# Performance work log

Hardware: AMD Instinct MI355X
Metric: run time of the kernel (lower is better)

## Reference

```python
import jax, jax.numpy as jnp
import numpy as np

K = 9          # neighbors per node (loop=False)
BN_EPS = 1e-5  # BatchNorm2d eps


def setup_inputs() -> dict:
    key = jax.random.key(0)
    k1, k2, k3 = jax.random.split(key, 3)
    B, C, H, W_ = 16, 384, 32, 32
    x = jax.random.normal(k1, (B, C, H, W_), dtype=jnp.float32)
    # GCNConv linear weight (PyG stores [out, in]; y = x @ W.T) and bias
    Wg = jax.random.normal(k2, (C, C), dtype=jnp.float32) / np.sqrt(C)
    bg = jax.random.normal(k3, (C,), dtype=jnp.float32) * 0.02
    gamma = jnp.ones((C,), dtype=jnp.float32)
    beta = jnp.zeros((C,), dtype=jnp.float32)
    return {"x": x, "Wg": Wg, "bg": bg, "gamma": gamma, "beta": beta}


def _knn_indices(xn):
    # xn: [B, N, C] -> neighbor indices [B, N, K] (self excluded)
    sq = jnp.sum(xn * xn, axis=-1)                       # [B, N]
    d = sq[:, :, None] + sq[:, None, :] - 2.0 * jnp.einsum("bnc,bmc->bnm", xn, xn)
    N = xn.shape[1]
    d = d + jnp.eye(N, dtype=xn.dtype) * jnp.finfo(xn.dtype).max  # exclude self
    _, nbr = jax.lax.top_k(-d, K)                        # [B, N, K]
    return nbr


def reference(x, Wg, bg, gamma, beta):
    B, C, H, W_ = x.shape
    N = H * W_
    BN_nodes = B * N
    shortcut = x

    # Flatten to nodes: [B*N, C]
    xn = jnp.transpose(x, (0, 2, 3, 1)).reshape(B, N, C)

    # Per-graph kNN in feature space (PyG knn_graph, flow source_to_target:
    # edges from neighbor (src) to query node (dst))
    nbr = _knn_indices(xn)                                # [B, N, K]
    offs = (jnp.arange(B) * N)[:, None, None]             # [B,1,1]
    src = (nbr + offs).reshape(-1)                        # [B*N*K]
    dst = jnp.broadcast_to(jnp.arange(N)[None, :, None] + offs, (B, N, K)).reshape(-1)

    # GCNConv: add self loops, symmetric normalization
    loops = jnp.arange(BN_nodes)
    src = jnp.concatenate([src, loops])
    dst = jnp.concatenate([dst, loops])

    xw = xn.reshape(BN_nodes, C) @ Wg.T                   # node-wise linear

    deg = jax.ops.segment_sum(jnp.ones_like(dst, dtype=xw.dtype), dst, num_segments=BN_nodes)
    dinv = jax.lax.rsqrt(deg)                             # deg >= 1 due to self loops
    norm = dinv[src] * dinv[dst]                          # [E]

    out = jax.ops.segment_sum(norm[:, None] * xw[src], dst, num_segments=BN_nodes) + bg

    # Back to B x C x H x W
    out = jnp.transpose(out.reshape(B, H, W_, C), (0, 3, 1, 2))

    # BatchNorm2d (training-mode batch statistics, biased variance)
    mu = jnp.mean(out, axis=(0, 2, 3), keepdims=True)
    var = jnp.mean((out - mu) ** 2, axis=(0, 2, 3), keepdims=True)
    out = gamma[None, :, None, None] * (out - mu) * jax.lax.rsqrt(var + BN_EPS) + beta[None, :, None, None]

    # GELU + residual (drop_path = 0 -> identity)
    out = jax.nn.gelu(out) + shortcut
    return out
```

## Files before the change

### kernel.cpp

```cpp
#include <hip/hip_runtime.h>
#include <math.h>

#define B_ 16
#define C_ 384
#define N_ 1024
#define K_ 9

typedef _Float16 f16x8 __attribute__((ext_vector_type(8)));
typedef _Float16 f16x4 __attribute__((ext_vector_type(4)));
typedef float f32x4 __attribute__((ext_vector_type(4)));
typedef unsigned long long u64;

__device__ __forceinline__ void gld_lds16(const void* g, void* l) {
  __builtin_amdgcn_global_load_lds((const __attribute__((address_space(1))) void*)g,
                                   (__attribute__((address_space(3))) void*)l, 16, 0, 0);
}

__global__ __launch_bounds__(256) void k_cvt(const float* __restrict__ x,
                                             const float* __restrict__ Wg,
                                             ushort* __restrict__ xhT, ushort* __restrict__ xlT,
                                             float* __restrict__ sq, ushort* __restrict__ WgH,
                                             ushort* __restrict__ WgL,
                                             float* __restrict__ stats) {
  const int bid = blockIdx.x;
  const int t = threadIdx.x;
  if (bid >= 512) {
    const int i = ((bid - 512) * 256 + t) * 4;
    float4 v = *(const float4*)(Wg + i);
    float vv[4] = {v.x, v.y, v.z, v.w};
    f16x4 hv, lv;
#pragma unroll
    for (int j = 0; j < 4; ++j) {
      _Float16 h = (_Float16)vv[j];
      hv[j] = h;
      lv[j] = (_Float16)(vv[j] - (float)h);
    }
    *(f16x4*)(WgH + i) = hv;
    *(f16x4*)(WgL + i) = lv;
    if (bid == 512) {
      stats[t] = 0.f;
      stats[t + 256] = 0.f;
      stats[t + 512] = 0.f;
    }
    return;
  }
  const int b = bid >> 5, n0 = (bid & 31) * 32;
  __shared__ float ld[384 * 33];
  {
    const int cb = t >> 2, j8 = (t & 3) * 8;
#pragma unroll
    for (int i = 0; i < 6; ++i) {
      const int c = i * 64 + cb;
      const float* src = x + ((size_t)(b * C_ + c) * N_ + n0 + j8);
      float4 v0 = *(const float4*)src;
      float4 v1 = *(const float4*)(src + 4);
      float* dst = &ld[c * 33 + j8];
      dst[0] = v0.x; dst[1] = v0.y; dst[2] = v0.z; dst[3] = v0.w;
      dst[4] = v1.x; dst[5] = v1.y; dst[6] = v1.z; dst[7] = v1.w;
    }
  }
  __syncthreads();
  {
    const int n = t >> 3, l = t & 7;
#pragma unroll
    for (int i = 0; i < 6; ++i) {
      const int c8 = i * 64 + l * 8;
      f16x8 hv, lv;
#pragma unroll
      for (int j = 0; j < 8; ++j) {
        float v = ld[(c8 + j) * 33 + n];
        _Float16 h = (_Float16)v;
        hv[j] = h;
        lv[j] = (_Float16)(v - (float)h);
      }
      const size_t off = (size_t)(b * N_ + n0 + n) * C_ + c8;
      *(f16x8*)(xhT + off) = hv;
      *(f16x8*)(xlT + off) = lv;
    }
    double s = 0.0;
    const int cbase = l * 48;
#pragma unroll
    for (int cc = 0; cc < 48; ++cc) {
      float v = ld[(cbase + cc) * 33 + n];
      s = fma((double)v, (double)v, s);
    }
    s += __shfl_xor(s, 1, 64);
    s += __shfl_xor(s, 2, 64);
    s += __shfl_xor(s, 4, 64);
    if (l == 0) sq[b * N_ + n0 + n] = (float)s;
  }
}

__device__ __forceinline__ void ce2f(float& a, float& b) {
  float lo = fminf(a, b), hi = fmaxf(a, b);
  a = lo;
  b = hi;
}
__device__ __forceinline__ void ce9u(u64& a, u64& b) {
  u64 lo = a < b ? a : b;
  u64 hi = a < b ? b : a;
  a = lo;
  b = hi;
}
__device__ __forceinline__ void mrg9(float* a, const float* b) {
  float m[9];
#pragma unroll
  for (int k = 0; k < 9; ++k) m[k] = fminf(a[k], b[8 - k]);
  ce2f(m[0], m[8]);
  ce2f(m[1], m[5]); ce2f(m[2], m[6]); ce2f(m[3], m[7]); ce2f(m[4], m[8]);
  ce2f(m[1], m[3]); ce2f(m[2], m[4]); ce2f(m[5], m[7]); ce2f(m[6], m[8]);
  ce2f(m[1], m[2]); ce2f(m[3], m[4]); ce2f(m[5], m[6]); ce2f(m[7], m[8]);
#pragma unroll
  for (int k = 0; k < 9; ++k) a[k] = m[k];
}

__global__ __launch_bounds__(256, 2) void k_gx(const ushort* __restrict__ xhT,
                                               const ushort* __restrict__ xlT,
                                               const float* __restrict__ sq,
                                               u64* __restrict__ part,
                                               const ushort* __restrict__ WgH,
                                               const ushort* __restrict__ WgL,
                                               float* __restrict__ xw) {
  __shared__ alignas(16) char sm[2][32768];
  const int bid = blockIdx.x;
  const int t = threadIdx.x;
  const int lane = t & 63, wid = t >> 6, quad = lane >> 4, lrow = lane & 15;
  const int wr = wid >> 1, wc = wid & 1;
  const int lrow4 = lane >> 2, lpos = lane & 3;

  if (bid >= 576) {
    const int bid2 = bid - 576;
    const int xcd = bid2 & 7, j = bid2 >> 3;
    const int pair = xcd * 16 + j / 6;
    const int ct = j % 6;
    const int b = pair >> 3, nt = pair & 7;
    const int co0 = ct * 64, n0 = nt * 128;
    char* smbase = &sm[0][0];

    f32x4 acc[2][4];
#pragma unroll
    for (int mi = 0; mi < 2; ++mi)
#pragma unroll
      for (int ni = 0; ni < 4; ++ni) acc[mi][ni] = (f32x4){0.f, 0.f, 0.f, 0.f};

    const char* asrc[2] = {(const char*)(WgH + (size_t)co0 * C_),
                           (const char*)(WgL + (size_t)co0 * C_)};
    const char* bsrc[2] = {(const char*)(xhT + (size_t)(b * N_ + n0) * C_),
                           (const char*)(xlT + (size_t)(b * N_ + n0) * C_)};

    auto stage = [&](int it) {
      char* dst = smbase + (it & 1) * 24576;
      const int ktB = it * 64;
#pragma unroll
      for (int i = 0; i < 6; ++i) {
        const int c = wid * 6 + i;
        const char* src;
        int base, row;
        if (c < 8) {
          const int arr = c >> 2, sub = c & 3;
          src = asrc[arr];
          base = arr * 4096 + sub * 1024;
          row = sub * 16 + lrow4;
        } else {
          const int cc = c - 8, arr = cc >> 3, sub = cc & 7;
          src = bsrc[arr];
          base = 8192 + arr * 8192 + sub * 1024;
          row = sub * 16 + lrow4;
        }
        const int swz = lpos ^ ((row >> 1) & 3);
        gld_lds16(src + (size_t)row * 768 + ktB + swz * 16, dst + base + lane * 16);
      }
    };

    stage(0);
    for (int it = 0; it < 12; ++it) {
      __syncthreads();
      if (it < 11) stage(it + 1);
      const char* smb = smbase + (it & 1) * 24576;
      f16x8 bh[4], bl[4];
#pragma unroll
      for (int ni = 0; ni < 4; ++ni) {
        const int row = wr * 64 + ni * 16 + lrow;
        const int off = row * 64 + (quad ^ ((row >> 1) & 3)) * 16;
        bh[ni] = *(const f16x8*)(smb + 8192 + off);
        bl[ni] = *(const f16x8*)(smb + 16384 + off);
      }
#pragma unroll
      for (int mi = 0; mi < 2; ++mi) {
        const int row = wc * 32 + mi * 16 + lrow;
        const int off = row * 64 + (quad ^ ((row >> 1) & 3)) * 16;
        f16x8 ah = *(const f16x8*)(smb + off);
        f16x8 al = *(const f16x8*)(smb + 4096 + off);
#pragma unroll
        for (int ni = 0; ni < 4; ++ni) {
          acc[mi][ni] = __builtin_amdgcn_mfma_f32_16x16x32_f16(ah, bh[ni], acc[mi][ni], 0, 0, 0);
          acc[mi][ni] = __builtin_amdgcn_mfma_f32_16x16x32_f16(al, bh[ni], acc[mi][ni], 0, 0, 0);
          acc[mi][ni] = __builtin_amdgcn_mfma_f32_16x16x32_f16(ah, bl[ni], acc[mi][ni], 0, 0, 0);
        }
      }
    }
#pragma unroll
    for (int mi = 0; mi < 2; ++mi)
#pragma unroll
      for (int ni = 0; ni < 4; ++ni)
#pragma unroll
        for (int r = 0; r < 4; ++r) {
          const int c_g = co0 + wc * 32 + mi * 16 + quad * 4 + r;
          const int n_g = n0 + wr * 64 + ni * 16 + lrow;
          xw[((size_t)b * C_ + c_g) * N_ + n_g] = acc[mi][ni][r];
        }
    return;
  }

  const int xcd = bid & 7, j = bid >> 3;
  const int b_local = xcd * 2 + j / 36;
  int pid = j % 36;
  int rt = 0, off0 = 0;
  while (pid >= off0 + (8 - rt)) {
    off0 += 8 - rt;
    ++rt;
  }
  const int mt = rt + (pid - off0);
  const int b = b_local;
  const int n0 = rt * 128, m0 = mt * 128;

  const char* src = (const char*)((wid & 1) ? xlT : xhT) +
                    (size_t)(b * N_ + ((wid >> 1) ? m0 : n0)) * C_ * 2;

  f32x4 acc[4][4];
#pragma unroll
  for (int mi = 0; mi < 4; ++mi)
#pragma unroll
    for (int ni = 0; ni < 4; ++ni) acc[mi][ni] = (f32x4){0.f, 0.f, 0.f, 0.f};

  auto stage = [&](int it) {
    char* dst = sm[it & 1] + wid * 8192;
    const int ktB = it * 64;
#pragma unroll
    for (int i = 0; i < 8; ++i) {
      const int row = i * 16 + lrow4;
      const int swz = lpos ^ ((row >> 1) & 3);
      gld_lds16(src + (size_t)row * 768 + ktB + swz * 16, dst + i * 1024 + lane * 16);
    }
  };

  stage(0);
  for (int it = 0; it < 12; ++it) {
    __syncthreads();
    if (it < 11) stage(it + 1);
    const char* smb = sm[it & 1];
    f16x8 ah[4], al[4];
#pragma unroll
    for (int mi = 0; mi < 4; ++mi) {
      const int row = wr * 64 + mi * 16 + lrow;
      const int off = row * 64 + (quad ^ ((row >> 1) & 3)) * 16;
      ah[mi] = *(const f16x8*)(smb + off);
      al[mi] = *(const f16x8*)(smb + 8192 + off);
    }
#pragma unroll
    for (int ni = 0; ni < 4; ++ni) {
      const int row = wc * 64 + ni * 16 + lrow;
      const int off = row * 64 + (quad ^ ((row >> 1) & 3)) * 16;
      f16x8 bh = *(const f16x8*)(smb + 16384 + off);
      f16x8 bl = *(const f16x8*)(smb + 24576 + off);
#pragma unroll
      for (int mi = 0; mi < 4; ++mi) {
        acc[mi][ni] = __builtin_amdgcn_mfma_f32_16x16x32_f16(bh, ah[mi], acc[mi][ni], 0, 0, 0);
        acc[mi][ni] = __builtin_amdgcn_mfma_f32_16x16x32_f16(bh, al[mi], acc[mi][ni], 0, 0, 0);
        acc[mi][ni] = __builtin_amdgcn_mfma_f32_16x16x32_f16(bl, ah[mi], acc[mi][ni], 0, 0, 0);
      }
    }
  }
  __syncthreads();

  const float* sqb = sq + b * N_;
  float sqm_[4][4];
#pragma unroll
  for (int ni = 0; ni < 4; ++ni)
#pragma unroll
    for (int r = 0; r < 4; ++r) sqm_[ni][r] = sqb[m0 + wc * 64 + ni * 16 + quad * 4 + r];
  float sqq_[4];
#pragma unroll
  for (int mi = 0; mi < 4; ++mi) sqq_[mi] = sqb[n0 + wr * 64 + mi * 16 + lrow];

  float* smf = (float*)sm;
#pragma unroll
  for (int mi = 0; mi < 4; ++mi) {
    const int qL = wr * 64 + mi * 16 + lrow;
    const int qG = n0 + qL;
#pragma unroll
    for (int ni = 0; ni < 4; ++ni) {
      const int tc = wc * 16 + ni * 4 + quad;
      const int stv = tc ^ (qL & 31);
      f32x4 dv;
#pragma unroll
      for (int r = 0; r < 4; ++r) {
        const int mG = m0 + wc * 64 + ni * 16 + quad * 4 + r;
        float d = fmaf(-2.f, acc[mi][ni][r], sqq_[mi] + sqm_[ni][r]);
        if (mG == qG) d = 3.402823466e38f;
        dv[r] = d;
      }
      *(f32x4*)(smf + qL * 128 + stv * 4) = dv;
    }
  }
  __syncthreads();

  const int half = lane >> 5;
  float kA[9], kB[9], kC[9], kD[9];

  {
    const int qsel = wid * 32 + (lane & 31);
#pragma unroll
    for (int k = 0; k < 9; ++k) kA[k] = kB[k] = kC[k] = kD[k] = 3.402823466e38f;
    auto ins16 = [&](float* key, int tcb) {
#pragma unroll
      for (int i = 0; i < 4; ++i) {
        const int tc = tcb + i;
        const int stv = tc ^ (qsel & 31);
        f32x4 q4 = *(const f32x4*)(smf + qsel * 128 + stv * 4);
#pragma unroll
        for (int e = 0; e < 4; ++e) {
          key[8] = fminf(key[8], q4[e]);
#pragma unroll
          for (int s = 8; s >= 1; --s) ce2f(key[s - 1], key[s]);
        }
      }
    };
    ins16(kA, half * 16 + 0);
    ins16(kB, half * 16 + 4);
    ins16(kC, half * 16 + 8);
    ins16(kD, half * 16 + 12);
    mrg9(kA, kB);
    mrg9(kC, kD);
    mrg9(kA, kC);
    {
      float pk[9];
#pragma unroll
      for (int k = 0; k < 9; ++k) pk[k] = __shfl_xor(kA[k], 32, 64);
      mrg9(kA, pk);
    }
    const float v9 = kA[8];
    int c_lt = 0;
#pragma unroll
    for (int k = 0; k < 8; ++k) c_lt += (kA[k] < v9) ? 1 : 0;

    u64 lt_mask = 0ull, eq_mask = 0ull;
#pragma unroll
    for (int i = 0; i < 16; ++i) {
      const int tc = half * 16 + i;
      const int stv = tc ^ (qsel & 31);
      f32x4 q4 = *(const f32x4*)(smf + qsel * 128 + stv * 4);
#pragma unroll
      for (int e = 0; e < 4; ++e) {
        const int jj = i * 4 + e;
        lt_mask |= (q4[e] < v9) ? (1ull << jj) : 0ull;
        eq_mask |= (q4[e] == v9) ? (1ull << jj) : 0ull;
      }
    }
    const int ltc = __popcll(lt_mask), eqc = __popcll(eq_mask);
    const int packed = ltc | (eqc << 16);
    const int other = __shfl_xor(packed, 32, 64);
    const int lt_pref = half ? (other & 0xFFFF) : 0;
    const int eq_pref = half ? (other >> 16) : 0;

    u64* pp = part + (((size_t)(b_local * 8 + mt) * N_) + (n0 + qsel)) * 9;
    int slot = lt_pref;
    u64 msk = lt_mask;
    while (msk) {
      const int jj = __builtin_ctzll(msk);
      msk &= msk - 1;
      const int mL = half * 64 + jj;
      const int stv = (mL >> 2) ^ (qsel & 31);
      const float val = smf[qsel * 128 + stv * 4 + (mL & 3)];
      unsigned fb = __float_as_uint(val);
      unsigned mono = (fb >> 31) ? ~fb : (fb | 0x80000000u);
      pp[slot++] = ((u64)mono << 32) | (unsigned)(m0 + mL);
    }
    unsigned fb9 = __float_as_uint(v9);
    unsigned mono9 = (fb9 >> 31) ? ~fb9 : (fb9 | 0x80000000u);
    slot = c_lt + eq_pref;
    msk = eq_mask;
    while (msk && slot < 9) {
      const int jj = __builtin_ctzll(msk);
      msk &= msk - 1;
      pp[slot++] = ((u64)mono9 << 32) | (unsigned)(m0 + half * 64 + jj);
    }
  }

  if (rt != mt) {
    const int msel = wid * 32 + (lane & 31);
    const int mlo = msel & 3, mhi = msel >> 2;
#pragma unroll
    for (int k = 0; k < 9; ++k) kA[k] = kB[k] = kC[k] = kD[k] = 3.402823466e38f;
    auto insCol = [&](float* key, int q0) {
#pragma unroll
      for (int i = 0; i < 16; ++i) {
        const int qL = q0 + i;
        const float v = smf[qL * 128 + ((mhi ^ (qL & 31)) << 2) + mlo];
        key[8] = fminf(key[8], v);
#pragma unroll
        for (int s = 8; s >= 1; --s) ce2f(key[s - 1], key[s]);
      }
    };
    insCol(kA, half * 64 + 0);
    insCol(kB, half * 64 + 16);
    insCol(kC, half * 64 + 32);
    insCol(kD, half * 64 + 48);
    mrg9(kA, kB);
    mrg9(kC, kD);
    mrg9(kA, kC);
    {
      float pk[9];
#pragma unroll
      for (int k = 0; k < 9; ++k) pk[k] = __shfl_xor(kA[k], 32, 64);
      mrg9(kA, pk);
    }
    const float v9 = kA[8];
    int c_lt = 0;
#pragma unroll
    for (int k = 0; k < 8; ++k) c_lt += (kA[k] < v9) ? 1 : 0;

    u64 lt_mask = 0ull, eq_mask = 0ull;
#pragma unroll
    for (int jj = 0; jj < 64; ++jj) {
      const int qL = half * 64 + jj;
      const float v = smf[qL * 128 + ((mhi ^ (qL & 31)) << 2) + mlo];
      lt_mask |= (v < v9) ? (1ull << jj) : 0ull;
      eq_mask |= (v == v9) ? (1ull << jj) : 0ull;
    }
    const int ltc = __popcll(lt_mask), eqc = __popcll(eq_mask);
    const int packed = ltc | (eqc << 16);
    const int other = __shfl_xor(packed, 32, 64);
    const int lt_pref = half ? (other & 0xFFFF) : 0;
    const int eq_pref = half ? (other >> 16) : 0;

    u64* pp = part + (((size_t)(b_local * 8 + rt) * N_) + (m0 + msel)) * 9;
    int slot = lt_pref;
    u64 msk = lt_mask;
    while (msk) {
      const int jj = __builtin_ctzll(msk);
      msk &= msk - 1;
      const int qL = half * 64 + jj;
      const float val = smf[qL * 128 + ((mhi ^ (qL & 31)) << 2) + mlo];
      unsigned fb = __float_as_uint(val);
      unsigned mono = (fb >> 31) ? ~fb : (fb | 0x80000000u);
      pp[slot++] = ((u64)mono << 32) | (unsigned)(n0 + qL);
    }
    unsigned fb9 = __float_as_uint(v9);
    unsigned mono9 = (fb9 >> 31) ? ~fb9 : (fb9 | 0x80000000u);
    slot = c_lt + eq_pref;
    msk = eq_mask;
    while (msk && slot < 9) {
      const int jj = __builtin_ctzll(msk);
      msk &= msk - 1;
      pp[slot++] = ((u64)mono9 << 32) | (unsigned)(n0 + half * 64 + jj);
    }
  }
}

__global__ void k_mrg(const u64* __restrict__ part, int* __restrict__ nbr, int base_node) {
  const int nl = blockIdx.x * 256 + threadIdx.x;
  const int bl = nl >> 10, q = nl & 1023;
  const u64* p = part + ((size_t)(bl * 8) * N_ + q) * 9;
  u64 key[9];
#pragma unroll
  for (int k = 0; k < 9; ++k) key[k] = ~0ull;
#pragma unroll
  for (int seg = 0; seg < 8; ++seg) {
    const u64* ps = p + (size_t)seg * N_ * 9;
#pragma unroll
    for (int k9 = 0; k9 < 9; ++k9) {
      u64 kk = ps[k9];
      key[8] = key[8] < kk ? key[8] : kk;
#pragma unroll
      for (int s = 8; s >= 1; --s) ce9u(key[s - 1], key[s]);
    }
  }
  int* np = nbr + (size_t)(base_node + nl) * K_;
#pragma unroll
  for (int k = 0; k < 9; ++k) np[k] = (int)(unsigned)(key[k] & 0xFFFFFFFFu);
}

__global__ __launch_bounds__(256) void k_agg(const float* __restrict__ xw,
                                             const int* __restrict__ nbr,
                                             const float* __restrict__ bg,
                                             float* __restrict__ out,
                                             float* __restrict__ stats) {
  const int ct = blockIdx.x % (C_ / 8);
  const int b = blockIdx.x / (C_ / 8);
  const int c0 = ct * 8;
  __shared__ alignas(16) int nb_l[N_ * K_];
  __shared__ alignas(16) float row_l[8][N_ + 4];
  __shared__ float red[2][8][4];
  const int tid = threadIdx.x;
  const int4* gp = (const int4*)(nbr + (size_t)b * N_ * K_);
  int4* lp = (int4*)nb_l;
  for (int t = tid; t < N_ * K_ / 4; t += 256) lp[t] = gp[t];
  for (int t = tid; t < 8 * (N_ / 4); t += 256) {
    const int j = t >> 8, n4 = t & 255;
    float4 v = ((const float4*)(xw + ((size_t)(b * C_ + c0 + j)) * N_))[n4];
    *(float4*)&row_l[j][n4 * 4] = v;
  }
  __syncthreads();
  float bgc[8];
#pragma unroll
  for (int j = 0; j < 8; ++j) bgc[j] = bg[c0 + j];
  float s1[8], s2[8];
#pragma unroll
  for (int j = 0; j < 8; ++j) {
    s1[j] = 0.f;
    s2[j] = 0.f;
  }
  float* outb = out + ((size_t)b * C_ + c0) * N_;
#pragma unroll
  for (int s = 0; s < 4; ++s) {
    const int n = tid + 256 * s;
    const int* nn_ = &nb_l[n * K_];
    int idx[K_];
#pragma unroll
    for (int k = 0; k < K_; ++k) idx[k] = nn_[k];
    float a[8];
#pragma unroll
    for (int j = 0; j < 8; ++j) a[j] = row_l[j][n];
#pragma unroll
    for (int k = 0; k < K_; ++k) {
      const int m = idx[k];
#pragma unroll
      for (int j = 0; j < 8; ++j) a[j] += row_l[j][m];
    }
#pragma unroll
    for (int j = 0; j < 8; ++j) {
      float y = fmaf(a[j], 0.099999994f, bgc[j]);
      outb[(size_t)j * N_ + n] = y;
      s1[j] += y;
      s2[j] = fmaf(y, y, s2[j]);
    }
  }
#pragma unroll
  for (int off = 32; off > 0; off >>= 1)
#pragma unroll
    for (int j = 0; j < 8; ++j) {
      s1[j] += __shfl_down(s1[j], off, 64);
      s2[j] += __shfl_down(s2[j], off, 64);
    }
  const int lane = tid & 63, wid = tid >> 6;
  if (lane == 0)
#pragma unroll
    for (int j = 0; j < 8; ++j) {
      red[0][j][wid] = s1[j];
      red[1][j][wid] = s2[j];
    }
  __syncthreads();
  if (tid < 16) {
    const int j = tid & 7, which = tid >> 3;
    float v = red[which][j][0] + red[which][j][1] + red[which][j][2] + red[which][j][3];
    atomicAdd(&stats[which * C_ + c0 + j], v);
  }
}

__global__ void k_bn(const float* __restrict__ x, const float* __restrict__ gamma,
                     const float* __restrict__ beta, const float* __restrict__ stats,
                     float* __restrict__ out) {
  const int f = blockIdx.x * blockDim.x + threadIdx.x;
  const int e = f * 4;
  const int c = (e >> 10) % C_;
  const float inv = 1.f / 16384.f;
  const float mu = stats[c] * inv;
  const float var = fmaf(-mu, mu, stats[C_ + c] * inv);
  const float sc = gamma[c] * rsqrtf(var + 1e-5f);
  const float sh = fmaf(-mu, sc, beta[c]);
  float4 y = ((const float4*)out)[f];
  float4 xv = ((const float4*)x)[f];
  auto gl = [](float z) {
    float z3 = z * z * z;
    float t = 0.7978845608028654f * fmaf(0.044715f, z3, z);
    float th = tanhf(t);
    return 0.5f * z * (1.f + th);
  };
  float4 o;
  o.x = gl(fmaf(y.x, sc, sh)) + xv.x;
  o.y = gl(fmaf(y.y, sc, sh)) + xv.y;
  o.z = gl(fmaf(y.z, sc, sh)) + xv.z;
  o.w = gl(fmaf(y.w, sc, sh)) + xv.w;
  ((float4*)out)[f] = o;
}

extern "C" void kernel_launch(void* const* d_in, const int* in_sizes, int n_in,
                              void* d_out, int out_size, void* d_ws, size_t ws_size,
                              hipStream_t stream) {
  const float* x = (const float*)d_in[0];
  const float* Wg = (const float*)d_in[1];
  const float* bg = (const float*)d_in[2];
  const float* gamma = (const float*)d_in[3];
  const float* beta = (const float*)d_in[4];
  float* out = (float*)d_out;

  char* ws = (char*)d_ws;
  ushort* xhT = (ushort*)ws;
  ushort* xlT = (ushort*)(ws + 12582912);
  ushort* WgH = (ushort*)(ws + 25165824);
  ushort* WgL = (ushort*)(ws + 25460736);
  float* sq = (float*)(ws + 25755648);
  u64* part = (u64*)(ws + 25821184);
  float* xw = (float*)(ws + 25821184);
  part = (u64*)(ws + 25821184);
  xw = (float*)(ws + 25821184 + 9437184);
  int* nbr = (int*)(ws + 25821184 + 9437184 + 25165824);
  float* stats = (float*)(ws + 25821184 + 9437184 + 25165824 + 589824);

  k_cvt<<<656, 256, 0, stream>>>(x, Wg, xhT, xlT, sq, WgH, WgL, stats);
  k_gx<<<1344, 256, 0, stream>>>(xhT, xlT, sq, part, WgH, WgL, xw);
  k_mrg<<<64, 256, 0, stream>>>(part, nbr, 0);
  k_agg<<<B_ * (C_ / 8), 256, 0, stream>>>(xw, nbr, bg, out, stats);
  k_bn<<<6144, 256, 0, stream>>>(x, gamma, beta, stats, out);
}
```

Before: 214.3 us.

## Split fused gram/xw kernel into separate launches and reorder gram tile schedule

The combined kernel that ran both the kNN Gram tiles and the node-wise linear GEMM under one grid is split into two kernels. The linear GEMM now uses a smaller LDS footprint (48KB) and launch bounds of 3 blocks per CU, so it is no longer limited by the 64KB allocation the Gram path needs. The Gram tile mapping is reordered so off-diagonal tiles are scheduled before diagonal ones. The cost is an extra launch and the loss of overlap between the two heterogeneous workloads within one grid.

```diff
diff --git a/kernel.cpp b/kernel.cpp
--- a/kernel.cpp
+++ b/kernel.cpp
@@ -114,13 +114,10 @@
   for (int k = 0; k < 9; ++k) a[k] = m[k];
 }
 
-__global__ __launch_bounds__(256, 2) void k_gx(const ushort* __restrict__ xhT,
-                                               const ushort* __restrict__ xlT,
-                                               const float* __restrict__ sq,
-                                               u64* __restrict__ part,
-                                               const ushort* __restrict__ WgH,
-                                               const ushort* __restrict__ WgL,
-                                               float* __restrict__ xw) {
+__global__ __launch_bounds__(256, 2) void k_gram(const ushort* __restrict__ xhT,
+                                                 const ushort* __restrict__ xlT,
+                                                 const float* __restrict__ sq,
+                                                 u64* __restrict__ part) {
   __shared__ alignas(16) char sm[2][32768];
   const int bid = blockIdx.x;
   const int t = threadIdx.x;
@@ -128,99 +125,22 @@
   const int wr = wid >> 1, wc = wid & 1;
   const int lrow4 = lane >> 2, lpos = lane & 3;
 
-  if (bid >= 576) {
-    const int bid2 = bid - 576;
-    const int xcd = bid2 & 7, j = bid2 >> 3;
-    const int pair = xcd * 16 + j / 6;
-    const int ct = j % 6;
-    const int b = pair >> 3, nt = pair & 7;
-    const int co0 = ct * 64, n0 = nt * 128;
-    char* smbase = &sm[0][0];
-
-    f32x4 acc[2][4];
-#pragma unroll
-    for (int mi = 0; mi < 2; ++mi)
-#pragma unroll
-      for (int ni = 0; ni < 4; ++ni) acc[mi][ni] = (f32x4){0.f, 0.f, 0.f, 0.f};
-
-    const char* asrc[2] = {(const char*)(WgH + (size_t)co0 * C_),
-                           (const char*)(WgL + (size_t)co0 * C_)};
-    const char* bsrc[2] = {(const char*)(xhT + (size_t)(b * N_ + n0) * C_),
-                           (const char*)(xlT + (size_t)(b * N_ + n0) * C_)};
-
-    auto stage = [&](int it) {
-      char* dst = smbase + (it & 1) * 24576;
-      const int ktB = it * 64;
-#pragma unroll
-      for (int i = 0; i < 6; ++i) {
-        const int c = wid * 6 + i;
-        const char* src;
-        int base, row;
-        if (c < 8) {
-          const int arr = c >> 2, sub = c & 3;
-          src = asrc[arr];
-          base = arr * 4096 + sub * 1024;
-          row = sub * 16 + lrow4;
-        } else {
-          const int cc = c - 8, arr = cc >> 3, sub = cc & 7;
-          src = bsrc[arr];
-          base = 8192 + arr * 8192 + sub * 1024;
-          row = sub * 16 + lrow4;
-        }
-        const int swz = lpos ^ ((row >> 1) & 3);
-        gld_lds16(src + (size_t)row * 768 + ktB + swz * 16, dst + base + lane * 16);
-      }
-    };
-
-    stage(0);
-    for (int it = 0; it < 12; ++it) {
-      __syncthreads();
-      if (it < 11) stage(it + 1);
-      const char* smb = smbase + (it & 1) * 24576;
-      f16x8 bh[4], bl[4];
-#pragma unroll
-      for (int ni = 0; ni < 4; ++ni) {
-        const int row = wr * 64 + ni * 16 + lrow;
-        const int off = row * 64 + (quad ^ ((row >> 1) & 3)) * 16;
-        bh[ni] = *(const f16x8*)(smb + 8192 + off);
-        bl[ni] = *(const f16x8*)(smb + 16384 + off);
-      }
-#pragma unroll
-      for (int mi = 0; mi < 2; ++mi) {
-        const int row = wc * 32 + mi * 16 + lrow;
-        const int off = row * 64 + (quad ^ ((row >> 1) & 3)) * 16;
-        f16x8 ah = *(const f16x8*)(smb + off);
-        f16x8 al = *(const f16x8*)(smb + 4096 + off);
-#pragma unroll
-        for (int ni = 0; ni < 4; ++ni) {
-          acc[mi][ni] = __builtin_amdgcn_mfma_f32_16x16x32_f16(ah, bh[ni], acc[mi][ni], 0, 0, 0);
-          acc[mi][ni] = __builtin_amdgcn_mfma_f32_16x16x32_f16(al, bh[ni], acc[mi][ni], 0, 0, 0);
-          acc[mi][ni] = __builtin_amdgcn_mfma_f32_16x16x32_f16(ah, bl[ni], acc[mi][ni], 0, 0, 0);
-        }
-      }
-    }
-#pragma unroll
-    for (int mi = 0; mi < 2; ++mi)
-#pragma unroll
-      for (int ni = 0; ni < 4; ++ni)
-#pragma unroll
-        for (int r = 0; r < 4; ++r) {
-          const int c_g = co0 + wc * 32 + mi * 16 + quad * 4 + r;
-          const int n_g = n0 + wr * 64 + ni * 16 + lrow;
-          xw[((size_t)b * C_ + c_g) * N_ + n_g] = acc[mi][ni][r];
-        }
-    return;
-  }
-
   const int xcd = bid & 7, j = bid >> 3;
   const int b_local = xcd * 2 + j / 36;
-  int pid = j % 36;
-  int rt = 0, off0 = 0;
-  while (pid >= off0 + (8 - rt)) {
-    off0 += 8 - rt;
-    ++rt;
-  }
-  const int mt = rt + (pid - off0);
+  const int pid = j % 36;
+  int rt, mt;
+  if (pid < 28) {
+    int idx = pid, off0 = 0;
+    rt = 0;
+    while (idx >= off0 + (7 - rt)) {
+      off0 += 7 - rt;
+      ++rt;
+    }
+    mt = rt + 1 + (idx - off0);
+  } else {
+    rt = pid - 28;
+    mt = rt;
+  }
   const int b = b_local;
   const int n0 = rt * 128, m0 = mt * 128;
 
@@ -456,6 +376,97 @@
       pp[slot++] = ((u64)mono9 << 32) | (unsigned)(n0 + half * 64 + jj);
     }
   }
+}
+
+__global__ __launch_bounds__(256, 3) void k_xw(const ushort* __restrict__ xhT,
+                                               const ushort* __restrict__ xlT,
+                                               const ushort* __restrict__ WgH,
+                                               const ushort* __restrict__ WgL,
+                                               float* __restrict__ xw) {
+  const int bid = blockIdx.x;
+  const int xcd = bid & 7, j = bid >> 3;
+  const int pair = xcd * 16 + j / 6;
+  const int ct = j % 6;
+  const int b = pair >> 3, nt = pair & 7;
+  const int co0 = ct * 64, n0 = nt * 128;
+  __shared__ alignas(16) char sm[2][24576];
+  const int t = threadIdx.x;
+  const int lane = t & 63, wid = t >> 6, quad = lane >> 4, lrow = lane & 15;
+  const int wr = wid >> 1, wc = wid & 1;
+  const int lrow4 = lane >> 2, lpos = lane & 3;
+
+  f32x4 acc[2][4];
+#pragma unroll
+  for (int mi = 0; mi < 2; ++mi)
+#pragma unroll
+    for (int ni = 0; ni < 4; ++ni) acc[mi][ni] = (f32x4){0.f, 0.f, 0.f, 0.f};
+
+  const char* asrc[2] = {(const char*)(WgH + (size_t)co0 * C_),
+                         (const char*)(WgL + (size_t)co0 * C_)};
+  const char* bsrc[2] = {(const char*)(xhT + (size_t)(b * N_ + n0) * C_),
+                         (const char*)(xlT + (size_t)(b * N_ + n0) * C_)};
+
+  auto stage = [&](int it) {
+    char* dst = sm[it & 1];
+    const int ktB = it * 64;
+#pragma unroll
+    for (int i = 0; i < 6; ++i) {
+      const int c = wid * 6 + i;
+      const char* src;
+      int base, row;
+      if (c < 8) {
+        const int arr = c >> 2, sub = c & 3;
+        src = asrc[arr];
+        base = arr * 4096 + sub * 1024;
+        row = sub * 16 + lrow4;
+      } else {
+        const int cc = c - 8, arr = cc >> 3, sub = cc & 7;
+        src = bsrc[arr];
+        base = 8192 + arr * 8192 + sub * 1024;
+        row = sub * 16 + lrow4;
+      }
+      const int swz = lpos ^ ((row >> 1) & 3);
+      gld_lds16(src + (size_t)row * 768 + ktB + swz * 16, dst + base + lane * 16);
+    }
+  };
+
+  stage(0);
+  for (int it = 0; it < 12; ++it) {
+    __syncthreads();
+    if (it < 11) stage(it + 1);
+    const char* smb = sm[it & 1];
+    f16x8 bh[4], bl[4];
+#pragma unroll
+    for (int ni = 0; ni < 4; ++ni) {
+      const int row = wr * 64 + ni * 16 + lrow;
+      const int off = row * 64 + (quad ^ ((row >> 1) & 3)) * 16;
+      bh[ni] = *(const f16x8*)(smb + 8192 + off);
+      bl[ni] = *(const f16x8*)(smb + 16384 + off);
+    }
+#pragma unroll
+    for (int mi = 0; mi < 2; ++mi) {
+      const int row = wc * 32 + mi * 16 + lrow;
+      const int off = row * 64 + (quad ^ ((row >> 1) & 3)) * 16;
+      f16x8 ah = *(const f16x8*)(smb + off);
+      f16x8 al = *(const f16x8*)(smb + 4096 + off);
+#pragma unroll
+      for (int ni = 0; ni < 4; ++ni) {
+        acc[mi][ni] = __builtin_amdgcn_mfma_f32_16x16x32_f16(ah, bh[ni], acc[mi][ni], 0, 0, 0);
+        acc[mi][ni] = __builtin_amdgcn_mfma_f32_16x16x32_f16(al, bh[ni], acc[mi][ni], 0, 0, 0);
+        acc[mi][ni] = __builtin_amdgcn_mfma_f32_16x16x32_f16(ah, bl[ni], acc[mi][ni], 0, 0, 0);
+      }
+    }
+  }
+#pragma unroll
+  for (int mi = 0; mi < 2; ++mi)
+#pragma unroll
+    for (int ni = 0; ni < 4; ++ni)
+#pragma unroll
+      for (int r = 0; r < 4; ++r) {
+        const int c_g = co0 + wc * 32 + mi * 16 + quad * 4 + r;
+        const int n_g = n0 + wr * 64 + ni * 16 + lrow;
+        xw[((size_t)b * C_ + c_g) * N_ + n_g] = acc[mi][ni][r];
+      }
 }
 
 __global__ void k_mrg(const u64* __restrict__ part, int* __restrict__ nbr, int base_node) {
@@ -602,14 +613,13 @@
   ushort* WgL = (ushort*)(ws + 25460736);
   float* sq = (float*)(ws + 25755648);
   u64* part = (u64*)(ws + 25821184);
-  float* xw = (float*)(ws + 25821184);
-  part = (u64*)(ws + 25821184);
-  xw = (float*)(ws + 25821184 + 9437184);
+  float* xw = (float*)(ws + 25821184 + 9437184);
   int* nbr = (int*)(ws + 25821184 + 9437184 + 25165824);
   float* stats = (float*)(ws + 25821184 + 9437184 + 25165824 + 589824);
 
   k_cvt<<<656, 256, 0, stream>>>(x, Wg, xhT, xlT, sq, WgH, WgL, stats);
-  k_gx<<<1344, 256, 0, stream>>>(xhT, xlT, sq, part, WgH, WgL, xw);
+  k_gram<<<576, 256, 0, stream>>>(xhT, xlT, sq, part);
+  k_xw<<<768, 256, 0, stream>>>(xhT, xlT, WgH, WgL, xw);
   k_mrg<<<64, 256, 0, stream>>>(part, nbr, 0);
   k_agg<<<B_ * (C_ / 8), 256, 0, stream>>>(xw, nbr, bg, out, stats);
   k_bn<<<6144, 256, 0, stream>>>(x, gamma, beta, stats, out);
```

Measured after the change: 213.9 us. About the same (-0.2%).
